# Kernel tuning notes

Measured on AMD Instinct MI355X. Metric: run time of the kernel, lower is better.

## Reference

```python
import jax, jax.numpy as jnp
import numpy as np

BATCH = 16384
MAZE_LEN = 3844  # 31*31*4
P = 0.0          # init kwarg p (default)
CLAMP_MIN = float(np.exp(-90.0))

# is_f(maze,row,col,tile) = maze[4*col + 124*row + tile]
IDX_A = 4 * 1 + 124 * 0 + 2    # is_f(maze, 0, 1, 2)  -> 6
IDX_B = 4 * 29 + 124 * 30 + 3  # is_f(maze, 30, 29, 3) -> 3839

def _chain_indices():
    idx = []
    for i in range(31):
        idx.append(124 * i + 1)    # is_f(maze, i, 0, 1)
        idx.append(124 * i + 121)  # is_f(maze, i, 30, 1)
    for i in range(28):
        idx.append(4 * (i + 2) + 1)   # is_f(maze, 0, i+2, 1)
        idx.append(4 * i + 3721)      # is_f(maze, 30, i, 1)
    return np.asarray(idx, dtype=np.int32)

CHAIN_IDX = jnp.asarray(_chain_indices())  # [118]

def _and_f(x, y, p):
    # Hamacher fuzzy AND: x*y / (p + (1-p)*(x+y-x*y)).
    # (original has a 0/0 guard only for x==y==p==0; inputs are in (0,1) here)
    denom = p + (1.0 - p) * (x + y - x * y)
    return x * y / denom

def setup_inputs() -> dict:
    key = jax.random.key(0)
    maze = jax.random.uniform(key, (BATCH, MAZE_LEN), dtype=jnp.float32)
    return {"maze": maze}

def reference(maze) -> jnp.ndarray:
    p = P
    # initial AND of the two special tiles
    result = _and_f(maze[:, IDX_A], maze[:, IDX_B], p)  # [B]
    vals = maze[:, CHAIN_IDX]  # [B, 118] gathered chain operands
    def step(carry, v):  # carry: [B], v: [B]
        return _and_f(carry, v, p), None
    result, _ = jax.lax.scan(step, result, vals.T)  # sequential per-element, vectorized over batch
    clamped = jnp.clip(result, CLAMP_MIN)
    return jnp.mean(-jnp.log(clamped))
```

## Files before the change

kernel.cpp:

```cpp
#include <hip/hip_runtime.h>
#include <math.h>

#define BATCH    16384
#define MAZE_LEN 3844
#define NIDX     120
#define NBLOCKS  (BATCH / 4)

struct IdxTable { int v[128]; };

static constexpr IdxTable make_idx() {
    IdxTable a{};
    int n = 0;
    a.v[n++] = 4 * 1 + 124 * 0 + 2;
    a.v[n++] = 4 * 29 + 124 * 30 + 3;
    for (int i = 0; i < 31; ++i) { a.v[n++] = 124 * i + 1; a.v[n++] = 124 * i + 121; }
    for (int i = 0; i < 28; ++i) { a.v[n++] = 4 * (i + 2) + 1; a.v[n++] = 4 * i + 3721; }
    for (int i = 1; i < NIDX; ++i) {
        int key = a.v[i]; int j = i - 1;
        while (j >= 0 && a.v[j] > key) { a.v[j + 1] = a.v[j]; --j; }
        a.v[j + 1] = key;
    }
    for (int i = NIDX; i < 128; ++i) a.v[i] = 0;
    return a;
}

__constant__ IdxTable c_idx = make_idx();

__global__ __launch_bounds__(256) void fuzzy_rows(
        const float* __restrict__ maze, float* __restrict__ partial) {
    const int lane = threadIdx.x & 63;
    const int wave = threadIdx.x >> 6;
    const int row  = (blockIdx.x << 2) | wave;

    const float* rp = maze + (size_t)row * MAZE_LEN;

    const int c0 = c_idx.v[lane];
    const int c1 = c_idx.v[64 + lane];

    const float x0 = rp[c0];
    const float x1 = rp[c1];

    float t = 1.0f / x0 - 1.0f;
    const float t1 = 1.0f / x1 - 1.0f;
    if (lane < NIDX - 64) t += t1;

    #pragma unroll
    for (int off = 32; off > 0; off >>= 1)
        t += __shfl_xor(t, off, 64);

    __shared__ float s_part[4];
    if (lane == 0)
        s_part[wave] = fminf(log1pf(t), 90.0f);
    __syncthreads();

    if (threadIdx.x == 0)
        partial[blockIdx.x] = s_part[0] + s_part[1] + s_part[2] + s_part[3];
}

__global__ __launch_bounds__(256) void reduce_partials(
        const float* __restrict__ partial, float* __restrict__ out) {
    float t = 0.0f;
    #pragma unroll
    for (int i = 0; i < NBLOCKS / 256; ++i)
        t += partial[threadIdx.x + (i << 8)];

    #pragma unroll
    for (int off = 32; off > 0; off >>= 1)
        t += __shfl_xor(t, off, 64);

    __shared__ float s_part[4];
    if ((threadIdx.x & 63) == 0)
        s_part[threadIdx.x >> 6] = t;
    __syncthreads();

    if (threadIdx.x == 0)
        out[0] = (s_part[0] + s_part[1] + s_part[2] + s_part[3])
                 * (1.0f / (float)BATCH);
}

extern "C" void kernel_launch(void* const* d_in, const int* in_sizes, int n_in,
                              void* d_out, int out_size, void* d_ws, size_t ws_size,
                              hipStream_t stream) {
    const float* maze = (const float*)d_in[0];
    float* out  = (float*)d_out;
    float* part = (float*)d_ws;

    fuzzy_rows<<<dim3(NBLOCKS), dim3(256), 0, stream>>>(maze, part);
    reduce_partials<<<dim3(1), dim3(256), 0, stream>>>(part, out);
}
```

Before: 297.3 us.

## Replace sparse per-row gather with dense float4 streaming and weighted reciprocal sum

Instead of each wave gathering the 120 scattered operands of one row, every block now streams full rows with coalesced float4 loads. A constant weight table marks which maze positions are used; unused slots are biased by 1e30 so their reciprocal contributes nothing. Each block handles 8 rows, reducing each row with wave shuffles and shared memory before the log. This trades scattered, latency-bound accesses for reading the whole input contiguously, which multiplies the bytes read. It also switches to the approximate hardware reciprocal, which slightly changes numerics.

```diff
diff --git a/kernel.cpp b/kernel.cpp
--- a/kernel.cpp
+++ b/kernel.cpp
@@ -3,74 +3,98 @@
 
 #define BATCH    16384
 #define MAZE_LEN 3844
-#define NIDX     120
-#define NBLOCKS  (BATCH / 4)
+#define NCHUNK   961
+#define ROWS_PER_BLOCK 8
+#define NBLK1    (BATCH / ROWS_PER_BLOCK)
+#define NTERMS   120.0f
 
-struct IdxTable { int v[128]; };
 
-static constexpr IdxTable make_idx() {
-    IdxTable a{};
-    int n = 0;
-    a.v[n++] = 4 * 1 + 124 * 0 + 2;
-    a.v[n++] = 4 * 29 + 124 * 30 + 3;
-    for (int i = 0; i < 31; ++i) { a.v[n++] = 124 * i + 1; a.v[n++] = 124 * i + 121; }
-    for (int i = 0; i < 28; ++i) { a.v[n++] = 4 * (i + 2) + 1; a.v[n++] = 4 * i + 3721; }
-    for (int i = 1; i < NIDX; ++i) {
-        int key = a.v[i]; int j = i - 1;
-        while (j >= 0 && a.v[j] > key) { a.v[j + 1] = a.v[j]; --j; }
-        a.v[j + 1] = key;
-    }
-    for (int i = NIDX; i < 128; ++i) a.v[i] = 0;
-    return a;
+struct WTab { float w[1024][4]; };
+
+static constexpr WTab make_w() {
+    WTab t{};
+    int W[MAZE_LEN] = {};
+    W[4 * 1 + 124 * 0 + 2]  += 1;
+    W[4 * 29 + 124 * 30 + 3] += 1;
+    for (int i = 0; i < 31; ++i) { W[124 * i + 1] += 1; W[124 * i + 121] += 1; }
+    for (int i = 0; i < 28; ++i) { W[4 * (i + 2) + 1] += 1; W[4 * i + 3721] += 1; }
+    for (int c = 0; c < NCHUNK; ++c)
+        for (int j = 0; j < 4; ++j) t.w[c][j] = (float)W[4 * c + j];
+    return t;
 }
 
-__constant__ IdxTable c_idx = make_idx();
+__constant__ WTab c_w = make_w();
 
 __global__ __launch_bounds__(256) void fuzzy_rows(
         const float* __restrict__ maze, float* __restrict__ partial) {
-    const int lane = threadIdx.x & 63;
-    const int wave = threadIdx.x >> 6;
-    const int row  = (blockIdx.x << 2) | wave;
+    const int tid  = threadIdx.x;
+    const int lane = tid & 63;
+    const int wave = tid >> 6;
 
-    const float* rp = maze + (size_t)row * MAZE_LEN;
+    float4 w[4], B[4];
+    int off[4];
+    #pragma unroll
+    for (int k = 0; k < 4; ++k) {
+        const int c  = tid + (k << 8);
+        const int cc = (c < NCHUNK) ? c : (NCHUNK - 1);
+        off[k] = cc << 2;
+        const int wc = (c < NCHUNK) ? c : 1023;
+        w[k] = *(const float4*)&c_w.w[wc][0];
+        B[k].x = (w[k].x == 0.0f) ? 1e30f : 0.0f;
+        B[k].y = (w[k].y == 0.0f) ? 1e30f : 0.0f;
+        B[k].z = (w[k].z == 0.0f) ? 1e30f : 0.0f;
+        B[k].w = (w[k].w == 0.0f) ? 1e30f : 0.0f;
+    }
 
-    const int c0 = c_idx.v[lane];
-    const int c1 = c_idx.v[64 + lane];
+    __shared__ float s_part[4][ROWS_PER_BLOCK];
+    __shared__ float s_fin[ROWS_PER_BLOCK];
 
-    const float x0 = rp[c0];
-    const float x1 = rp[c1];
+    const float* rp = maze + (size_t)blockIdx.x * ROWS_PER_BLOCK * MAZE_LEN;
 
-    float t = 1.0f / x0 - 1.0f;
-    const float t1 = 1.0f / x1 - 1.0f;
-    if (lane < NIDX - 64) t += t1;
-
-    #pragma unroll
-    for (int off = 32; off > 0; off >>= 1)
-        t += __shfl_xor(t, off, 64);
-
-    __shared__ float s_part[4];
-    if (lane == 0)
-        s_part[wave] = fminf(log1pf(t), 90.0f);
+    for (int r = 0; r < ROWS_PER_BLOCK; ++r, rp += MAZE_LEN) {
+        float a0 = 0.0f, a1 = 0.0f, a2 = 0.0f, a3 = 0.0f;
+        #pragma unroll
+        for (int k = 0; k < 4; ++k) {
+            const float4 v = *(const float4*)(rp + off[k]);
+            a0 = fmaf(w[k].x, __builtin_amdgcn_rcpf(v.x + B[k].x), a0);
+            a1 = fmaf(w[k].y, __builtin_amdgcn_rcpf(v.y + B[k].y), a1);
+            a2 = fmaf(w[k].z, __builtin_amdgcn_rcpf(v.z + B[k].z), a2);
+            a3 = fmaf(w[k].w, __builtin_amdgcn_rcpf(v.w + B[k].w), a3);
+        }
+        float p = (a0 + a1) + (a2 + a3);
+        #pragma unroll
+        for (int o = 32; o > 0; o >>= 1) p += __shfl_xor(p, o, 64);
+        if (lane == 0) s_part[wave][r] = p;
+    }
     __syncthreads();
 
-    if (threadIdx.x == 0)
-        partial[blockIdx.x] = s_part[0] + s_part[1] + s_part[2] + s_part[3];
+    if (tid < ROWS_PER_BLOCK) {
+        const float S = s_part[0][tid] + s_part[1][tid]
+                      + s_part[2][tid] + s_part[3][tid] - NTERMS;
+        s_fin[tid] = fminf(log1pf(S), 90.0f);
+    }
+    __syncthreads();
+
+    if (tid == 0) {
+        float t = 0.0f;
+        #pragma unroll
+        for (int r = 0; r < ROWS_PER_BLOCK; ++r) t += s_fin[r];
+        partial[blockIdx.x] = t;
+    }
 }
 
 __global__ __launch_bounds__(256) void reduce_partials(
         const float* __restrict__ partial, float* __restrict__ out) {
     float t = 0.0f;
     #pragma unroll
-    for (int i = 0; i < NBLOCKS / 256; ++i)
+    for (int i = 0; i < NBLK1 / 256; ++i)
         t += partial[threadIdx.x + (i << 8)];
 
     #pragma unroll
-    for (int off = 32; off > 0; off >>= 1)
-        t += __shfl_xor(t, off, 64);
+    for (int o = 32; o > 0; o >>= 1) t += __shfl_xor(t, o, 64);
 
     __shared__ float s_part[4];
-    if ((threadIdx.x & 63) == 0)
-        s_part[threadIdx.x >> 6] = t;
+    if ((threadIdx.x & 63) == 0) s_part[threadIdx.x >> 6] = t;
     __syncthreads();
 
     if (threadIdx.x == 0)
@@ -85,6 +109,6 @@
     float* out  = (float*)d_out;
     float* part = (float*)d_ws;
 
-    fuzzy_rows<<<dim3(NBLOCKS), dim3(256), 0, stream>>>(maze, part);
+    fuzzy_rows<<<dim3(NBLK1), dim3(256), 0, stream>>>(maze, part);
     reduce_partials<<<dim3(1), dim3(256), 0, stream>>>(part, out);
 }
```

Measured after the change: 339.8 us. +14.3%, slower.
